# Optimization experiments

Hardware: AMD Instinct MI355X
Metric: run time of the kernel (lower is better)

The kernel has to match this reference:

```python
import jax, jax.numpy as jnp
import numpy as np

HIDDEN = 1024
N_HEADS = 16
HEAD_DIM = HIDDEN // N_HEADS
B, S = 4, 4096


def setup_inputs() -> dict:
    key = jax.random.key(0)
    k1, k2, k3, k4, k5 = jax.random.split(key, 5)
    hidden_states = jax.random.normal(k1, (B, S, HIDDEN), dtype=jnp.float32)
    attention_mask = jnp.zeros((B, 1, 1, S), dtype=jnp.float32)
    scale = 1.0 / np.sqrt(HIDDEN)
    Wq = jax.random.normal(k2, (HIDDEN, HIDDEN), dtype=jnp.float32) * scale
    bq = jax.random.normal(k3, (HIDDEN,), dtype=jnp.float32) * 0.01
    Wkv = jax.random.normal(k4, (HIDDEN, HIDDEN), dtype=jnp.float32) * scale
    bkv = jax.random.normal(k5, (HIDDEN,), dtype=jnp.float32) * 0.01
    return {"hidden_states": hidden_states, "attention_mask": attention_mask,
            "Wq": Wq, "bq": bq, "Wkv": Wkv, "bkv": bkv}


def _split_heads(x, b, s):
    # [B, S, HIDDEN] -> [B, H, S, D]
    return x.reshape(b, s, N_HEADS, HEAD_DIM).transpose(0, 2, 1, 3)


def reference(hidden_states, attention_mask, Wq, bq, Wkv, bkv):
    b, s, _ = hidden_states.shape
    inv_sqrt_d = 1.0 / np.sqrt(HEAD_DIM)

    q = _split_heads(hidden_states @ Wq + bq, b, s)     # [B,H,S,D]
    k = _split_heads(hidden_states @ Wkv + bkv, b, s)   # [B,H,S,D]; value == key

    # ---- global token (index 0) attends to everything ----
    gq = q[:, :, 0:1, :]                                              # [B,H,1,D]
    g_scores = jnp.einsum('bhqd,bhkd->bhqk', gq, k) * inv_sqrt_d + attention_mask
    g_attn = jax.nn.softmax(g_scores, axis=-1)                        # [B,H,1,S]
    g_vec = jnp.einsum('bhqk,bhkd->bhqd', g_attn, k)                  # [B,H,1,D]

    # ---- local tokens 1..S-1: keys = [self, global_vec, prev, next(wrap to 0)] ----
    k_self = k[:, :, 1:, :]                                           # [B,H,S-1,D]
    k_glob = jnp.broadcast_to(g_vec, k_self.shape)                    # [B,H,S-1,D]
    k_prev = k[:, :, :-1, :]                                          # [B,H,S-1,D]
    k_next = jnp.concatenate([k[:, :, 2:, :], k[:, :, 0:1, :]], axis=2)
    keys4 = jnp.stack([k_self, k_glob, k_prev, k_next], axis=-1)      # [B,H,S-1,D,4]

    l_scores = jnp.einsum('bhsd,bhsdk->bhsk', q[:, :, 1:, :], keys4) * inv_sqrt_d
    l_attn = jax.nn.softmax(l_scores, axis=-1)                        # [B,H,S-1,4]
    l_vec = jnp.einsum('bhsk,bhsdk->bhsd', l_attn, keys4)             # [B,H,S-1,D]

    context = jnp.concatenate([g_vec, l_vec], axis=2)                 # [B,H,S,D]
    context = context.transpose(0, 2, 1, 3).reshape(b, s, N_HEADS * HEAD_DIM)
    return context, l_attn[:, :, :, None, :]                          # [B,H,S-1,1,4]
```

## Files before the change

### kernel.cpp

```cpp
#include <hip/hip_runtime.h>
#include <hip/hip_bf16.h>

#define NHEADS 16
#define HDIM   64
#define HID    1024
#define BB     4
#define SS     4096
#define MM     (BB*SS)
#define KK     HID
#define NN     (2*HID)

using short8 = __attribute__((ext_vector_type(8))) short;
using f32x4  = __attribute__((ext_vector_type(4))) float;

__device__ __forceinline__ float bf2f(ushort u) {
  return __uint_as_float(((unsigned)u) << 16);
}
__device__ __forceinline__ ushort f2bf(float f) {
  unsigned u = __float_as_uint(f);
  unsigned r = (u + 0x7fffu + ((u >> 16) & 1u)) >> 16;
  return (ushort)r;
}

__device__ __forceinline__ void gload16(const void* g, void* l) {
  __builtin_amdgcn_global_load_lds(
      (const __attribute__((address_space(1))) void*)g,
      (__attribute__((address_space(3))) void*)l, 16, 0, 0);
}

__global__ __launch_bounds__(256) void cast_hs_k(const float* __restrict__ in,
                                                 ushort* __restrict__ out) {
  size_t i = ((size_t)blockIdx.x * 256 + threadIdx.x) * 8;
  float4 a = *(const float4*)(in + i);
  float4 b = *(const float4*)(in + i + 4);
  ushort r[8];
  r[0]=f2bf(a.x); r[1]=f2bf(a.y); r[2]=f2bf(a.z); r[3]=f2bf(a.w);
  r[4]=f2bf(b.x); r[5]=f2bf(b.y); r[6]=f2bf(b.z); r[7]=f2bf(b.w);
  *(uint4*)(out + i) = *(const uint4*)r;
}

__global__ __launch_bounds__(256) void wcast_k(const float* __restrict__ Wq,
                                               const float* __restrict__ Wkv,
                                               ushort* __restrict__ Bt) {
  __shared__ float tile[32][33];
  int k0 = blockIdx.x * 32, n0 = blockIdx.y * 32;
  int tx = threadIdx.x, ty = threadIdx.y;
  const float* src = (n0 < HID) ? Wq : Wkv;
  int nc = (n0 < HID) ? n0 : n0 - HID;
#pragma unroll
  for (int j = 0; j < 4; ++j)
    tile[ty + 8*j][tx] = src[(size_t)(k0 + ty + 8*j) * HID + nc + tx];
  __syncthreads();
#pragma unroll
  for (int j = 0; j < 4; ++j)
    Bt[(size_t)(n0 + ty + 8*j) * KK + k0 + tx] = f2bf(tile[tx][ty + 8*j]);
}

__global__ __launch_bounds__(512, 2) void gemm_k(const ushort* __restrict__ A,
                                                 const ushort* __restrict__ Bt,
                                                 const float* __restrict__ bq,
                                                 const float* __restrict__ bkv,
                                                 ushort* __restrict__ C) {
  extern __shared__ char lds_c[];
  const int tid = threadIdx.x;
  const int bid = blockIdx.x;
  const int wg = (bid & 7) * 64 + (bid >> 3);
  const int tm = wg >> 3, tn = wg & 7;
  const int w = tid >> 6, lane = tid & 63;
  const int wr = w >> 2, wc = w & 3;
  const int lr = lane & 15, hi = lane >> 4;

  const ushort* Ab = A  + (size_t)tm * 256 * KK;
  const ushort* Bb = Bt + (size_t)tn * 256 * KK;

  const int o0 = tid * 16;
  const int srow = tid >> 3;
  const int sc = tid & 7;
  const size_t aoff = (size_t)srow * KK + ((sc ^ (srow & 7)) << 3);

  const int swz0 = (hi ^ (lr & 7)) << 4;
  const int swz1 = ((4 + hi) ^ (lr & 7)) << 4;
  const int rowA = (wr * 128 + lr) * 128;
  const int rowB = (wc * 64 + lr) * 128;

  float biasv[4];
#pragma unroll
  for (int n = 0; n < 4; ++n) {
    int col = tn * 256 + wc * 64 + n * 16 + lr;
    biasv[n] = (col < HID) ? bq[col] : bkv[col - HID];
  }

  f32x4 acc[8][4];
#pragma unroll
  for (int M = 0; M < 8; ++M)
#pragma unroll
    for (int n = 0; n < 4; ++n) acc[M][n] = (f32x4){0.f, 0.f, 0.f, 0.f};
  short8 bfrag[4];

#define STG(PANEL, TILE, DST)                                                   \
  {                                                                             \
    const ushort* g0_ = (PANEL) + (TILE) * 64 + aoff;                           \
    gload16(g0_,         lds_c + (DST) + o0);                                   \
    gload16(g0_ + 65536, lds_c + (DST) + 8192 + o0);                            \
  }

#define LOADB(BUFB, SWZ)                                                        \
  _Pragma("unroll") for (int n = 0; n < 4; ++n)                                 \
    bfrag[n] = *(const short8*)(lds_c + (BUFB) + rowB + n * 2048 + (SWZ));

#define CPH(BUFA, MH, SWZ, STAGE_CODE, TAIL_CODE)                               \
  {                                                                             \
    short8 afrag[4];                                                            \
    _Pragma("unroll") for (int m = 0; m < 4; ++m)                               \
      afrag[m] = *(const short8*)(lds_c + (BUFA) + rowA + (MH) * 8192 +         \
                                  m * 2048 + (SWZ));                            \
    STAGE_CODE;                                                                 \
    __builtin_amdgcn_s_barrier();                                               \
    asm volatile("" ::: "memory");                                              \
    __builtin_amdgcn_s_setprio(1);                                              \
    _Pragma("unroll") for (int m = 0; m < 4; ++m)                               \
      _Pragma("unroll") for (int n = 0; n < 4; ++n)                             \
        acc[(MH) * 4 + m][n] = __builtin_amdgcn_mfma_f32_16x16x32_bf16(         \
            afrag[m], bfrag[n], acc[(MH) * 4 + m][n], 0, 0, 0);                 \
    __builtin_amdgcn_s_setprio(0);                                              \
    TAIL_CODE;                                                                  \
    __builtin_amdgcn_s_barrier();                                               \
    asm volatile("" ::: "memory");                                              \
  }

  STG(Bb,          0, 32768);
  STG(Bb + 131072, 0, 49152);
  STG(Ab,          0, 0);
  STG(Ab + 131072, 0, 16384);
  STG(Bb,          1, 98304);
  asm volatile("s_waitcnt vmcnt(2)" ::: "memory");
  __builtin_amdgcn_s_barrier();
  asm volatile("" ::: "memory");

#define ITER_BODY(T1, TN0, TN1, G, VM4)                                          \
  LOADB(32768, swz0);                                                            \
  CPH(0, 0, swz0, STG(Bb + 131072, (T1), 114688), {});                           \
  CPH(0, 1, swz0, STG(Ab, (T1), 65536), {});                                     \
  LOADB(32768, swz1);                                                            \
  CPH(0, 0, swz1, STG(Ab + 131072, (T1), 81920), {});                            \
  CPH(0, 1, swz1, { if (G) STG(Bb, (TN0), 32768) },                              \
      { asm volatile("s_waitcnt vmcnt(" #VM4 ")" ::: "memory");                  \
        __builtin_amdgcn_sched_barrier(0); });                                   \
  LOADB(98304, swz0);                                                            \
  CPH(65536, 0, swz0, { if (G) STG(Bb + 131072, (TN0), 49152) }, {});            \
  CPH(65536, 1, swz0, { if (G) STG(Ab, (TN0), 0) }, {});                         \
  LOADB(98304, swz1);                                                            \
  CPH(65536, 0, swz1, { if (G) STG(Ab + 131072, (TN0), 16384) }, {});            \
  CPH(65536, 1, swz1, { if (G) STG(Bb, (TN1), 98304) },                          \
      { asm volatile("s_waitcnt vmcnt(2)" ::: "memory");                         \
        __builtin_amdgcn_sched_barrier(0); });

  for (int it = 0; it < 7; ++it) {
    ITER_BODY(2 * it + 1, 2 * it + 2, 2 * it + 3, true, 2)
  }
  ITER_BODY(15, 0, 0, false, 0)

#undef ITER_BODY
#undef CPH
#undef LOADB
#undef STG

#pragma unroll
  for (int M = 0; M < 8; ++M) {
#pragma unroll
    for (int n = 0; n < 4; ++n) {
#pragma unroll
      for (int t = 0; t < 4; ++t) {
        int row = wr * 128 + M * 16 + hi * 4 + t;
        int col = wc * 64 + n * 16 + lr;
        *(ushort*)(lds_c + row * 512 + ((col * 2) ^ ((row & 7) << 4))) =
            f2bf(acc[M][n][t] + biasv[n]);
      }
    }
  }
  __syncthreads();
#pragma unroll
  for (int i = 0; i < 16; ++i) {
    int idx = i * 512 + tid;
    int row = idx >> 5, l = idx & 31;
    uint4 v = *(const uint4*)(lds_c + row * 512 + ((l ^ (row & 7)) << 4));
    *(uint4*)(C + (size_t)(tm * 256 + row) * NN + tn * 256 + l * 8) = v;
  }
}

#define GCH 8
#define GCS (SS / GCH)

__global__ __launch_bounds__(512) void gattn_part_k(const ushort* __restrict__ QK,
                                                    const float* __restrict__ mask,
                                                    float* __restrict__ P) {
  const int bh = blockIdx.x >> 3, c = blockIdx.x & 7;
  const int b = bh >> 4, h = bh & 15;
  const int tid = threadIdx.x, w = tid >> 6, lane = tid & 63;
  __shared__ float sc[GCS];
  __shared__ float red[8];
  __shared__ float vacc[8][64];

  const float gq = bf2f(QK[(size_t)b * SS * NN + h * HDIM + lane]);
  const int s0 = c * GCS;
  float mx = -1e30f;
  for (int s = w; s < GCS; s += 8) {
    float kv = bf2f(QK[((size_t)b * SS + s0 + s) * NN + HID + h * HDIM + lane]);
    float p = gq * kv;
#pragma unroll
    for (int o = 32; o; o >>= 1) p += __shfl_xor(p, o, 64);
    p = p * 0.125f + mask[b * SS + s0 + s];
    if (lane == 0) sc[s] = p;
    mx = fmaxf(mx, p);
  }
  if (lane == 0) red[w] = mx;
  __syncthreads();
  float bm = -1e30f;
#pragma unroll
  for (int i = 0; i < 8; ++i) bm = fmaxf(bm, red[i]);
  __syncthreads();
  float ls = 0.f;
  for (int s = tid; s < GCS; s += 512) {
    float e = __expf(sc[s] - bm);
    sc[s] = e;
    ls += e;
  }
#pragma unroll
  for (int o = 32; o; o >>= 1) ls += __shfl_xor(ls, o, 64);
  if (lane == 0) red[w] = ls;
  __syncthreads();
  float tot = 0.f;
#pragma unroll
  for (int i = 0; i < 8; ++i) tot += red[i];

  float a = 0.f;
  for (int s = w; s < GCS; s += 8)
    a += sc[s] * bf2f(QK[((size_t)b * SS + s0 + s) * NN + HID + h * HDIM + lane]);
  vacc[w][lane] = a;
  __syncthreads();
  if (w == 0) {
    float v = 0.f;
#pragma unroll
    for (int i = 0; i < 8; ++i) v += vacc[i][lane];
    P[1024 + (bh * 8 + c) * 64 + lane] = v;
    if (lane == 0) {
      P[bh * 8 + c] = bm;
      P[512 + bh * 8 + c] = tot;
    }
  }
}

__global__ __launch_bounds__(64) void gattn_comb_k(const float* __restrict__ P,
                                                   float* __restrict__ ctx,
                                                   float* __restrict__ gvec) {
  const int bh = blockIdx.x, b = bh >> 4, h = bh & 15;
  const int lane = threadIdx.x;
  float pm[8];
  float m = -1e30f;
#pragma unroll
  for (int c = 0; c < 8; ++c) { pm[c] = P[bh * 8 + c]; m = fmaxf(m, pm[c]); }
  float tot = 0.f, g = 0.f;
#pragma unroll
  for (int c = 0; c < 8; ++c) {
    float e = __expf(pm[c] - m);
    tot += P[512 + bh * 8 + c] * e;
    g += P[1024 + (bh * 8 + c) * 64 + lane] * e;
  }
  g /= tot;
  gvec[b * HID + h * HDIM + lane] = g;
  ctx[(size_t)b * SS * HID + h * HDIM + lane] = g;
}

__device__ __forceinline__ void unpack16(const ushort* __restrict__ p, float* f) {
  uint4 v0 = *(const uint4*)p;
  uint4 v1 = *(const uint4*)(p + 8);
  unsigned u[8] = {v0.x, v0.y, v0.z, v0.w, v1.x, v1.y, v1.z, v1.w};
#pragma unroll
  for (int i = 0; i < 8; ++i) {
    f[2*i]   = __uint_as_float(u[i] << 16);
    f[2*i+1] = __uint_as_float(u[i] & 0xffff0000u);
  }
}

__global__ __launch_bounds__(256) void local_attn_k(const ushort* __restrict__ QK,
                                                    const float* __restrict__ gvec,
                                                    float* __restrict__ out) {
  const int blk = blockIdx.x;
  const int b = blk >> 10;
  const int s = 1 + ((blk & 1023) << 2) + (int)(threadIdx.x >> 6);
  if (s >= SS) return;
  const int lane = threadIdx.x & 63;
  const int g = lane >> 2, j = lane & 3;
  const int db = g*HDIM + j*16;

  const size_t base = ((size_t)b*SS + s) * NN;
  const ushort* qp  = QK + base + db;
  const ushort* ksp = QK + base + HID + db;
  const ushort* kpp = QK + base - NN + HID + db;
  const int sn = (s == SS-1) ? 0 : s + 1;
  const ushort* knp = QK + ((size_t)b*SS + sn)*NN + HID + db;
  const float*  gvp = gvec + b*HID + db;

  float q[16], ks[16], kp[16], kn[16], gv[16];
  unpack16(qp, q); unpack16(ksp, ks); unpack16(kpp, kp); unpack16(knp, kn);
#pragma unroll
  for (int t = 0; t < 16; t += 4) *(float4*)(gv + t) = *(const float4*)(gvp + t);

  float d0=0.f, d1=0.f, d2=0.f, d3=0.f;
#pragma unroll
  for (int t = 0; t < 16; ++t) {
    d0 += q[t]*ks[t]; d1 += q[t]*gv[t]; d2 += q[t]*kp[t]; d3 += q[t]*kn[t];
  }
  d0 += __shfl_xor(d0, 1, 64); d0 += __shfl_xor(d0, 2, 64);
  d1 += __shfl_xor(d1, 1, 64); d1 += __shfl_xor(d1, 2, 64);
  d2 += __shfl_xor(d2, 1, 64); d2 += __shfl_xor(d2, 2, 64);
  d3 += __shfl_xor(d3, 1, 64); d3 += __shfl_xor(d3, 2, 64);

  float s0 = d0*0.125f, s1 = d1*0.125f, s2 = d2*0.125f, s3 = d3*0.125f;
  float m = fmaxf(fmaxf(s0, s1), fmaxf(s2, s3));
  float e0 = __expf(s0 - m), e1 = __expf(s1 - m), e2 = __expf(s2 - m), e3 = __expf(s3 - m);
  float inv = 1.f / (e0 + e1 + e2 + e3);
  float a0 = e0*inv, a1 = e1*inv, a2 = e2*inv, a3 = e3*inv;

  float o[16];
#pragma unroll
  for (int t = 0; t < 16; ++t) o[t] = a0*ks[t] + a1*gv[t] + a2*kp[t] + a3*kn[t];
  float* cp = out + ((size_t)b*SS + s)*HID + db;
#pragma unroll
  for (int t = 0; t < 16; t += 4) *(float4*)(cp + t) = *(const float4*)(o + t);

  if (j == 0) {
    float4 av; av.x = a0; av.y = a1; av.z = a2; av.w = a3;
    *(float4*)(out + (size_t)BB*SS*HID + (((size_t)b*NHEADS + g)*(SS-1) + (s-1))*4) = av;
  }
}

extern "C" void kernel_launch(void* const* d_in, const int* in_sizes, int n_in,
                              void* d_out, int out_size, void* d_ws, size_t ws_size,
                              hipStream_t stream) {
  const float* hs   = (const float*)d_in[0];
  const float* mask = (const float*)d_in[1];
  const float* Wq   = (const float*)d_in[2];
  const float* bq   = (const float*)d_in[3];
  const float* Wkv  = (const float*)d_in[4];
  const float* bkv  = (const float*)d_in[5];
  float* out = (float*)d_out;

  char* ws = (char*)d_ws;
  ushort* hsb  = (ushort*)ws;
  ushort* Bt   = (ushort*)(ws + 33554432);
  ushort* QK   = (ushort*)(ws + 33554432 + 4194304);
  float*  gvec = (float*)(ws + 33554432 + 4194304 + 67108864);
  float*  P    = (float*)(ws + 33554432 + 4194304 + 67108864 + 16384);

  cast_hs_k<<<MM*KK/(256*8), 256, 0, stream>>>(hs, hsb);
  wcast_k<<<dim3(KK/32, NN/32), dim3(32, 8), 0, stream>>>(Wq, Wkv, Bt);
  gemm_k<<<dim3((MM/256)*(NN/256)), dim3(512), 131072, stream>>>(hsb, Bt, bq, bkv, QK);
  gattn_part_k<<<BB*NHEADS*GCH, 512, 0, stream>>>(QK, mask, P);
  gattn_comb_k<<<BB*NHEADS, 64, 0, stream>>>(P, out, gvec);
  local_attn_k<<<BB*1024, 256, 0, stream>>>(QK, gvec, out);
}
```

Before: 170.0 us.

## Restructure GEMM pipeline into 32-wide K stages with transposed MFMA epilogue

Reworks the QKV GEMM main loop to stage 32-column K slices across four LDS buffers, with a new swizzle and deeper in-flight loads (vmcnt 8). It swaps the MFMA operand order so each lane holds four consecutive output columns. That lets the epilogue write bf16 results straight to global memory as packed 8-byte stores, dropping the LDS round trip and the __syncthreads. The aim is more load/compute overlap and a cheaper epilogue. In exchange the global stores are narrower and less coalesced, and there are more barriers per K step.

```diff
diff --git a/kernel.cpp b/kernel.cpp
--- a/kernel.cpp
+++ b/kernel.cpp
@@ -73,22 +73,14 @@
   const ushort* Ab = A  + (size_t)tm * 256 * KK;
   const ushort* Bb = Bt + (size_t)tn * 256 * KK;
 
-  const int o0 = tid * 16;
-  const int srow = tid >> 3;
-  const int sc = tid & 7;
-  const size_t aoff = (size_t)srow * KK + ((sc ^ (srow & 7)) << 3);
-
-  const int swz0 = (hi ^ (lr & 7)) << 4;
-  const int swz1 = ((4 + hi) ^ (lr & 7)) << 4;
-  const int rowA = (wr * 128 + lr) * 128;
-  const int rowB = (wc * 64 + lr) * 128;
-
-  float biasv[4];
-#pragma unroll
-  for (int n = 0; n < 4; ++n) {
-    int col = tn * 256 + wc * 64 + n * 16 + lr;
-    biasv[n] = (col < HID) ? bq[col] : bkv[col - HID];
-  }
+  const int d0 = tid * 16;
+  const int gch = (tid & 3) ^ ((tid >> 3) & 3);
+  const size_t soff0 = (size_t)(tid >> 2) * KK + gch * 8;
+  const size_t soff1 = soff0 + (size_t)128 * KK;
+
+  const int swz = (hi ^ ((lr >> 1) & 3)) << 4;
+  const int arow = (wr * 128 + lr) * 64 + swz;
+  const int brow = (wc * 64 + lr) * 64 + swz;
 
   f32x4 acc[8][4];
 #pragma unroll
@@ -97,23 +89,31 @@
     for (int n = 0; n < 4; ++n) acc[M][n] = (f32x4){0.f, 0.f, 0.f, 0.f};
   short8 bfrag[4];
 
-#define STG(PANEL, TILE, DST)                                                   \
+#define STG2(PANEL, KOFF)                                                       \
+                                            \
+  do {} while (0)
+
+#define STG(PANEL, KOFF, DSTB)                                                  \
   {                                                                             \
-    const ushort* g0_ = (PANEL) + (TILE) * 64 + aoff;                           \
-    gload16(g0_,         lds_c + (DST) + o0);                                   \
-    gload16(g0_ + 65536, lds_c + (DST) + 8192 + o0);                            \
-  }
-
-#define LOADB(BUFB, SWZ)                                                        \
+    const ushort* g_ = (PANEL) + (KOFF);                                        \
+    gload16(g_ + soff0, lds_c + (DSTB) + d0);                                   \
+    gload16(g_ + soff1, lds_c + (DSTB) + 8192 + d0);                            \
+  }
+
+#define LOADB(BBASE)                                                            \
   _Pragma("unroll") for (int n = 0; n < 4; ++n)                                 \
-    bfrag[n] = *(const short8*)(lds_c + (BUFB) + rowB + n * 2048 + (SWZ));
-
-#define CPH(BUFA, MH, SWZ, STAGE_CODE, TAIL_CODE)                               \
+    bfrag[n] = *(const short8*)(lds_c + (BBASE) + n * 1024 + brow);
+
+#define WAITV(N)                                                                \
+  { asm volatile("s_waitcnt vmcnt(" #N ")" ::: "memory");                       \
+    __builtin_amdgcn_sched_barrier(0); }
+
+#define PH(ABASE, MH, STAGE_CODE, TAIL_CODE)                                    \
   {                                                                             \
     short8 afrag[4];                                                            \
     _Pragma("unroll") for (int m = 0; m < 4; ++m)                               \
-      afrag[m] = *(const short8*)(lds_c + (BUFA) + rowA + (MH) * 8192 +         \
-                                  m * 2048 + (SWZ));                            \
+      afrag[m] = *(const short8*)(lds_c + (ABASE) + (MH) * 4096 +               \
+                                  m * 1024 + arow);                             \
     STAGE_CODE;                                                                 \
     __builtin_amdgcn_s_barrier();                                               \
     asm volatile("" ::: "memory");                                              \
@@ -121,70 +121,90 @@
     _Pragma("unroll") for (int m = 0; m < 4; ++m)                               \
       _Pragma("unroll") for (int n = 0; n < 4; ++n)                             \
         acc[(MH) * 4 + m][n] = __builtin_amdgcn_mfma_f32_16x16x32_bf16(         \
-            afrag[m], bfrag[n], acc[(MH) * 4 + m][n], 0, 0, 0);                 \
+            bfrag[n], afrag[m], acc[(MH) * 4 + m][n], 0, 0, 0);                 \
     __builtin_amdgcn_s_setprio(0);                                              \
     TAIL_CODE;                                                                  \
     __builtin_amdgcn_s_barrier();                                               \
     asm volatile("" ::: "memory");                                              \
   }
 
-  STG(Bb,          0, 32768);
-  STG(Bb + 131072, 0, 49152);
-  STG(Ab,          0, 0);
-  STG(Ab + 131072, 0, 16384);
-  STG(Bb,          1, 98304);
-  asm volatile("s_waitcnt vmcnt(2)" ::: "memory");
+  STG(Bb, 0,   32768);
+  STG(Ab, 0,   0);
+  STG(Bb, 32,  49152);
+  STG(Ab, 32,  16384);
+  STG(Bb, 64,  98304);
+  STG(Ab, 64,  65536);
+  WAITV(8)
   __builtin_amdgcn_s_barrier();
   asm volatile("" ::: "memory");
 
-#define ITER_BODY(T1, TN0, TN1, G, VM4)                                          \
-  LOADB(32768, swz0);                                                            \
-  CPH(0, 0, swz0, STG(Bb + 131072, (T1), 114688), {});                           \
-  CPH(0, 1, swz0, STG(Ab, (T1), 65536), {});                                     \
-  LOADB(32768, swz1);                                                            \
-  CPH(0, 0, swz1, STG(Ab + 131072, (T1), 81920), {});                            \
-  CPH(0, 1, swz1, { if (G) STG(Bb, (TN0), 32768) },                              \
-      { asm volatile("s_waitcnt vmcnt(" #VM4 ")" ::: "memory");                  \
-        __builtin_amdgcn_sched_barrier(0); });                                   \
-  LOADB(98304, swz0);                                                            \
-  CPH(65536, 0, swz0, { if (G) STG(Bb + 131072, (TN0), 49152) }, {});            \
-  CPH(65536, 1, swz0, { if (G) STG(Ab, (TN0), 0) }, {});                         \
-  LOADB(98304, swz1);                                                            \
-  CPH(65536, 0, swz1, { if (G) STG(Ab + 131072, (TN0), 16384) }, {});            \
-  CPH(65536, 1, swz1, { if (G) STG(Bb, (TN1), 98304) },                          \
-      { asm volatile("s_waitcnt vmcnt(2)" ::: "memory");                         \
-        __builtin_amdgcn_sched_barrier(0); });
+#define ITER(T1, T2, T3, W2, W4, W6, G)                                         \
+  LOADB(32768)                                                                  \
+  PH(0, 0, STG(Bb, (T1) * 64 + 32, 114688), {})                                 \
+  PH(0, 1, STG(Ab, (T1) * 64 + 32, 81920), WAITV(W2))                           \
+  LOADB(49152)                                                                  \
+  PH(16384, 0, { if (G) STG(Bb, (T2) * 64, 32768) }, {})                        \
+  PH(16384, 1, { if (G) STG(Ab, (T2) * 64, 0) }, WAITV(W4))                     \
+  LOADB(98304)                                                                  \
+  PH(65536, 0, { if (G) STG(Bb, (T2) * 64 + 32, 49152) }, {})                   \
+  PH(65536, 1, { if (G) STG(Ab, (T2) * 64 + 32, 16384) }, WAITV(W6))            \
+  LOADB(114688)                                                                 \
+  PH(81920, 0, { if (G) STG(Bb, (T3) * 64, 98304) }, {})                        \
+  PH(81920, 1, { if (G) STG(Ab, (T3) * 64, 65536) }, WAITV(0))
 
   for (int it = 0; it < 7; ++it) {
-    ITER_BODY(2 * it + 1, 2 * it + 2, 2 * it + 3, true, 2)
-  }
-  ITER_BODY(15, 0, 0, false, 0)
-
-#undef ITER_BODY
-#undef CPH
+    LOADB(32768)
+    PH(0, 0, STG(Bb, (2 * it + 1) * 64 + 32, 114688), {})
+    PH(0, 1, STG(Ab, (2 * it + 1) * 64 + 32, 81920), WAITV(8))
+    LOADB(49152)
+    PH(16384, 0, STG(Bb, (2 * it + 2) * 64, 32768), {})
+    PH(16384, 1, STG(Ab, (2 * it + 2) * 64, 0), WAITV(8))
+    LOADB(98304)
+    PH(65536, 0, STG(Bb, (2 * it + 2) * 64 + 32, 49152), {})
+    PH(65536, 1, STG(Ab, (2 * it + 2) * 64 + 32, 16384), WAITV(8))
+    LOADB(114688)
+    PH(81920, 0, STG(Bb, (2 * it + 3) * 64, 98304), {})
+    PH(81920, 1, STG(Ab, (2 * it + 3) * 64, 65536), WAITV(8))
+  }
+  LOADB(32768)
+  PH(0, 0, STG(Bb, 15 * 64 + 32, 114688), {})
+  PH(0, 1, STG(Ab, 15 * 64 + 32, 81920), WAITV(8))
+  LOADB(49152)
+  PH(16384, 0, {}, {})
+  PH(16384, 1, {}, WAITV(4))
+  LOADB(98304)
+  PH(65536, 0, {}, {})
+  PH(65536, 1, {}, WAITV(0))
+  LOADB(114688)
+  PH(81920, 0, {}, {})
+  PH(81920, 1, {}, {})
+
+#undef ITER
+#undef PH
+#undef WAITV
 #undef LOADB
 #undef STG
+#undef STG2
+
+  const float* bias = (tn < 4) ? (bq + tn * 256) : (bkv + (tn - 4) * 256);
+  float4 bv[4];
+#pragma unroll
+  for (int n = 0; n < 4; ++n)
+    bv[n] = *(const float4*)(bias + wc * 64 + n * 16 + hi * 4);
 
 #pragma unroll
   for (int M = 0; M < 8; ++M) {
+    size_t row = (size_t)tm * 256 + wr * 128 + M * 16 + lr;
+    ushort* cp = C + row * NN + tn * 256 + wc * 64 + hi * 4;
 #pragma unroll
     for (int n = 0; n < 4; ++n) {
-#pragma unroll
-      for (int t = 0; t < 4; ++t) {
-        int row = wr * 128 + M * 16 + hi * 4 + t;
-        int col = wc * 64 + n * 16 + lr;
-        *(ushort*)(lds_c + row * 512 + ((col * 2) ^ ((row & 7) << 4))) =
-            f2bf(acc[M][n][t] + biasv[n]);
-      }
+      unsigned p0 = (unsigned)f2bf(acc[M][n][0] + bv[n].x) |
+                    ((unsigned)f2bf(acc[M][n][1] + bv[n].y) << 16);
+      unsigned p1 = (unsigned)f2bf(acc[M][n][2] + bv[n].z) |
+                    ((unsigned)f2bf(acc[M][n][3] + bv[n].w) << 16);
+      uint2 st; st.x = p0; st.y = p1;
+      *(uint2*)(cp + n * 16) = st;
     }
-  }
-  __syncthreads();
-#pragma unroll
-  for (int i = 0; i < 16; ++i) {
-    int idx = i * 512 + tid;
-    int row = idx >> 5, l = idx & 31;
-    uint4 v = *(const uint4*)(lds_c + row * 512 + ((l ^ (row & 7)) << 4));
-    *(uint4*)(C + (size_t)(tm * 256 + row) * NN + tn * 256 + l * 8) = v;
   }
 }
 
```

After: 177.4 us. 4.4% more time.
